# Performance work log

Hardware: AMD Instinct MI355X
Metric: run time of the kernel (lower is better)

The kernel has to match this reference:

```python
import jax, jax.numpy as jnp
import numpy as np

EPS = 1e-7  # tf.keras.backend.epsilon()
DEGREE = 5
SCALE_BASE = 1.0
SCALE_LEGENDRE = 1.0


def legendre_basis(x, degree):
    # min/max normalization over the feature axis -> x_norm in [-1, 1]
    x_min = jnp.min(x, axis=-1, keepdims=True)
    x_max = jnp.max(x, axis=-1, keepdims=True)
    x_norm = 2.0 * (x - x_min) / (x_max - x_min + EPS) - 1.0
    polys = [jnp.ones_like(x_norm), x_norm]
    for n in range(2, degree + 1):
        p_n = ((2 * n - 1) * x_norm * polys[-1] - (n - 1) * polys[-2]) / n
        polys.append(p_n)
    return jnp.stack(polys, axis=-1)  # [b, i, degree+1]


def setup_inputs() -> dict:
    key = jax.random.key(0)
    k1, k2, k3 = jax.random.split(key, 3)
    b, i, o, d = 4096, 1024, 1024, DEGREE + 1
    x = jax.random.normal(k1, (b, i), dtype=jnp.float32)
    # HeUniform: limit = sqrt(6 / fan_in)
    lim_b = np.sqrt(6.0 / i)
    base_weight = jax.random.uniform(k2, (i, o), dtype=jnp.float32, minval=-lim_b, maxval=lim_b)
    legendre_weight = jax.random.uniform(k3, (i, o, d), dtype=jnp.float32, minval=-lim_b, maxval=lim_b)
    return {"x": x, "base_weight": base_weight, "legendre_weight": legendre_weight}


def reference(x, base_weight, legendre_weight):
    base_output = jax.nn.silu(x @ base_weight)  # [b, o]
    basis = legendre_basis(x, DEGREE)  # [b, i, d]
    # 'bi,iod,bid->bo' == fold x into the basis then contract (i, d)
    xb = x[..., None] * basis  # [b, i, d]
    legendre_output = jnp.einsum('bid,iod->bo', xb, legendre_weight)
    return SCALE_BASE * base_output + SCALE_LEGENDRE * legendre_output
```

## Files before the change

### kernel.cpp

```cpp
#include <hip/hip_runtime.h>
#include <stdint.h>

typedef unsigned short u16;
typedef unsigned int   u32;
typedef __attribute__((ext_vector_type(8)))  short bhalf8;
typedef __attribute__((ext_vector_type(16))) float f32x16;

#define B_ROWS 4096
#define I_DIM  1024
#define O_DIM  1024
#define N_D    6
#define K_LEG  (I_DIM * N_D)

#define BM 256
#define BN 256
#define BK 32
#define NU 56
#define SLOT_BYTES 32768
#define LDS_BYTES  131072

__device__ __forceinline__ u16 f2b(float f) {
  u32 u = __float_as_uint(f);
  return (u16)((u + 0x7fffu + ((u >> 16) & 1u)) >> 16);
}

__device__ __forceinline__ void gld_lds16(const void* g, void* l) {
  __builtin_amdgcn_global_load_lds(
      (const __attribute__((address_space(1))) u32*)(uintptr_t)g,
      (__attribute__((address_space(3))) u32*)(u32)(uintptr_t)l, 16, 0, 0);
}

#define RS 201
__global__ void k_prep_w(const float* __restrict__ bw, const float* __restrict__ lw,
                         u16* __restrict__ Bb, u16* __restrict__ Bl) {
  __shared__ float t[32 * RS];
  if (blockIdx.x < 1024) {
    const int bx = blockIdx.x & 31, by = blockIdx.x >> 5;
    const int i0 = by * 32, o0 = bx * 32;
    const int c = threadIdx.x & 31, r0 = threadIdx.x >> 5;
    #pragma unroll
    for (int k = 0; k < 4; ++k) {
      int r = r0 + k * 8;
      t[r * 33 + c] = bw[(size_t)(i0 + r) * O_DIM + o0 + c];
    }
    __syncthreads();
    #pragma unroll
    for (int k = 0; k < 4; ++k) {
      int r = r0 + k * 8;
      Bb[(size_t)(o0 + r) * I_DIM + i0 + c] = f2b(t[c * 33 + r]);
    }
  } else {
    const int blk = blockIdx.x - 1024;
    const int bx = blk & 31, by = blk >> 5;
    const int i0 = by * 32, o0 = bx * 32;
    for (int q = threadIdx.x; q < 32 * 48; q += 256) {
      int ri = q / 48, s4 = q % 48;
      float4 v = *(const float4*)(lw + (size_t)(i0 + ri) * (O_DIM * N_D) + o0 * N_D + s4 * 4);
      float* p = t + ri * RS + s4 * 4;
      p[0] = v.x; p[1] = v.y; p[2] = v.z; p[3] = v.w;
    }
    __syncthreads();
    for (int q = threadIdx.x; q < 32 * 96; q += 256) {
      int ro = q / 96, k = q % 96;
      int e0 = 2 * k, e1 = 2 * k + 1;
      float v0 = t[(e0 / 6) * RS + ro * 6 + (e0 % 6)];
      float v1 = t[(e1 / 6) * RS + ro * 6 + (e1 % 6)];
      u32* dst = (u32*)(Bl + (size_t)(o0 + ro) * K_LEG + i0 * N_D);
      dst[k] = (u32)f2b(v0) | ((u32)f2b(v1) << 16);
    }
  }
}

__global__ void k_prep_basis(const float* __restrict__ x,
                             u16* __restrict__ Ab, u16* __restrict__ Al) {
  int b = blockIdx.x;
  int t = threadIdx.x;
  float4 v = ((const float4*)(x + (size_t)b * I_DIM))[t];
  float mn = fminf(fminf(v.x, v.y), fminf(v.z, v.w));
  float mx = fmaxf(fmaxf(v.x, v.y), fmaxf(v.z, v.w));
  #pragma unroll
  for (int off = 32; off > 0; off >>= 1) {
    mn = fminf(mn, __shfl_xor(mn, off, 64));
    mx = fmaxf(mx, __shfl_xor(mx, off, 64));
  }
  __shared__ float smn[4], smx[4];
  if ((t & 63) == 0) { smn[t >> 6] = mn; smx[t >> 6] = mx; }
  __syncthreads();
  mn = fminf(fminf(smn[0], smn[1]), fminf(smn[2], smn[3]));
  mx = fmaxf(fmaxf(smx[0], smx[1]), fmaxf(smx[2], smx[3]));
  float sc = 2.0f / (mx - mn + 1e-7f);

  float xs[4] = {v.x, v.y, v.z, v.w};
  u32 lb[12];
  #pragma unroll
  for (int e = 0; e < 4; ++e) {
    float xv = xs[e];
    float xn = (xv - mn) * sc - 1.0f;
    float p0 = 1.0f, p1 = xn;
    float p2 = (3.0f * xn * p1 - 1.0f * p0) * (1.0f / 2.0f);
    float p3 = (5.0f * xn * p2 - 2.0f * p1) * (1.0f / 3.0f);
    float p4 = (7.0f * xn * p3 - 3.0f * p2) * (1.0f / 4.0f);
    float p5 = (9.0f * xn * p4 - 4.0f * p3) * (1.0f / 5.0f);
    lb[e * 3 + 0] = (u32)f2b(xv * p0) | ((u32)f2b(xv * p1) << 16);
    lb[e * 3 + 1] = (u32)f2b(xv * p2) | ((u32)f2b(xv * p3) << 16);
    lb[e * 3 + 2] = (u32)f2b(xv * p4) | ((u32)f2b(xv * p5) << 16);
  }
  u32 a0 = (u32)f2b(xs[0]) | ((u32)f2b(xs[1]) << 16);
  u32 a1 = (u32)f2b(xs[2]) | ((u32)f2b(xs[3]) << 16);
  *(uint2*)(Ab + (size_t)b * I_DIM + t * 4) = make_uint2(a0, a1);
  uint4* dl = (uint4*)(Al + (size_t)b * K_LEG + t * 24);
  dl[0] = make_uint4(lb[0], lb[1], lb[2], lb[3]);
  dl[1] = make_uint4(lb[4], lb[5], lb[6], lb[7]);
  dl[2] = make_uint4(lb[8], lb[9], lb[10], lb[11]);
}

__global__ __launch_bounds__(512, 2) void k_gemm(
    const u16* __restrict__ Ab, const u16* __restrict__ Bb,
    const u16* __restrict__ Al, const u16* __restrict__ Bl,
    float* __restrict__ out, float* __restrict__ P) {
  extern __shared__ char lds[];

  const int tid  = threadIdx.x;
  const int wave = tid >> 6;
  const int lane = tid & 63;
  const int wm = wave >> 2;
  const int wn = wave & 3;
  const u32 lr = lane & 31;
  const u32 hi = (u32)lane >> 5;

  const int bid   = blockIdx.x;
  const int bx    = bid >> 4;
  const int by    = (bid >> 2) & 3;
  const int split = bid & 3;
  const size_t brow = (size_t)bx * BM;
  const size_t bcol = (size_t)by * BN;
  const bool s0 = (split == 0);
  const int legbase = s0 ? 0 : (24 + 56 * (split - 1));

  const int r4 = tid >> 2;
  const size_t cs = (size_t)((((tid & 3) ^ ((r4 >> 1) & 3))) * 8);
  char* const l0 = lds + (u32)wave * 1024;

  const u16 *gA0, *gA1, *gB0, *gB1;
  auto set_ptrs = [&](const u16* A, const u16* Bt, size_t ldk, size_t kt) {
    const size_t ko = kt * BK + cs;
    gA0 = A  + (brow + r4) * ldk + ko;
    gA1 = A  + (brow + 128 + r4) * ldk + ko;
    gB0 = Bt + (bcol + r4) * ldk + ko;
    gB1 = Bt + (bcol + 128 + r4) * ldk + ko;
  };
  if (s0) set_ptrs(Ab, Bb, I_DIM, 0);
  else    set_ptrs(Al, Bl, K_LEG, (size_t)legbase);

  const u32 sxor   = (lr >> 1) & 3;
  const u32 chunk0 = ((0 + hi) ^ sxor) * 16;
  const u32 chunk1 = ((2 + hi) ^ sxor) * 16;
  const u32 abase_r = (u32)wm * 8192 + lr * 64;
  const u32 bbase_r = 16384u + ((u32)wn >> 1) * 8192 + ((u32)wn & 1) * 4096 + lr * 64;

  f32x16 acc[4][2] = {};
  bhalf8 af_[4], bf_[2];

  #pragma unroll
  for (int v = 0; v < 3; ++v) {
    char* d = l0 + (size_t)v * SLOT_BYTES;
    gld_lds16(gA0, d);          gld_lds16(gA1, d + 8192);
    gld_lds16(gB0, d + 16384);  gld_lds16(gB1, d + 24576);
    gA0 += BK; gA1 += BK; gB0 += BK; gB1 += BK;
  }
  asm volatile("s_waitcnt vmcnt(8)" ::: "memory");
  __builtin_amdgcn_s_barrier();

#define PH0(u, DO_STAGE) do {                                                 \
    const char* p_ = lds + (size_t)((u) & 3) * SLOT_BYTES;                    \
    _Pragma("unroll")                                                         \
    for (int n = 0; n < 2; ++n) bf_[n] = *(const bhalf8*)(p_ + bbase_r + n * 2048 + chunk0); \
    _Pragma("unroll")                                                         \
    for (int m = 0; m < 4; ++m) af_[m] = *(const bhalf8*)(p_ + abase_r + m * 2048 + chunk0); \
    if (DO_STAGE) {                                                           \
      char* d_ = l0 + (size_t)(((u) + 3) & 3) * SLOT_BYTES;                   \
      gld_lds16(gA0, d_); gld_lds16(gA1, d_ + 8192);                          \
    }                                                                         \
    asm volatile("" ::: "memory");                                            \
    __builtin_amdgcn_s_barrier();                                             \
    asm volatile("s_waitcnt lgkmcnt(0)" ::: "memory");                        \
    __builtin_amdgcn_sched_barrier(0);                                        \
    __builtin_amdgcn_s_setprio(1);                                            \
    _Pragma("unroll")                                                         \
    for (int m = 0; m < 4; ++m)                                               \
      _Pragma("unroll")                                                       \
      for (int n = 0; n < 2; ++n)                                             \
        acc[m][n] = __builtin_amdgcn_mfma_f32_32x32x16_bf16(af_[m], bf_[n], acc[m][n], 0, 0, 0); \
    __builtin_amdgcn_s_setprio(0);                                            \
    __builtin_amdgcn_s_barrier();                                             \
  } while (0)

#define PH1(u, DO_STAGE, VM) do {                                             \
    const char* p_ = lds + (size_t)((u) & 3) * SLOT_BYTES;                    \
    _Pragma("unroll")                                                         \
    for (int n = 0; n < 2; ++n) bf_[n] = *(const bhalf8*)(p_ + bbase_r + n * 2048 + chunk1); \
    _Pragma("unroll")                                                         \
    for (int m = 0; m < 4; ++m) af_[m] = *(const bhalf8*)(p_ + abase_r + m * 2048 + chunk1); \
    if (DO_STAGE) {                                                           \
      char* d_ = l0 + (size_t)(((u) + 3) & 3) * SLOT_BYTES;                   \
      gld_lds16(gB0, d_ + 16384); gld_lds16(gB1, d_ + 24576);                 \
      if (s0 && (u) + 4 == 32) set_ptrs(Al, Bl, K_LEG, 0);                    \
      else { gA0 += BK; gA1 += BK; gB0 += BK; gB1 += BK; }                    \
    }                                                                         \
    asm volatile("s_waitcnt vmcnt(" #VM ")" ::: "memory");                    \
    __builtin_amdgcn_s_barrier();                                             \
    asm volatile("s_waitcnt lgkmcnt(0)" ::: "memory");                        \
    __builtin_amdgcn_sched_barrier(0);                                        \
    __builtin_amdgcn_s_setprio(1);                                            \
    _Pragma("unroll")                                                         \
    for (int m = 0; m < 4; ++m)                                               \
      _Pragma("unroll")                                                       \
      for (int n = 0; n < 2; ++n)                                             \
        acc[m][n] = __builtin_amdgcn_mfma_f32_32x32x16_bf16(af_[m], bf_[n], acc[m][n], 0, 0, 0); \
    __builtin_amdgcn_s_setprio(0);                                            \
    __builtin_amdgcn_s_barrier();                                             \
  } while (0)

  for (int u = 0; u < NU - 3; ++u) {
    if (s0 && u == 32) {
      #pragma unroll
      for (int m = 0; m < 4; ++m)
        #pragma unroll
        for (int n = 0; n < 2; ++n)
          #pragma unroll
          for (int j = 0; j < 16; ++j) {
            float v = acc[m][n][j];
            acc[m][n][j] = v / (1.0f + __expf(-v));
          }
    }
    PH0(u, true);
    PH1(u, true, 8);
  }
  PH0(53, false); PH1(53, false, 4);
  PH0(54, false); PH1(54, false, 0);
  PH0(55, false); PH1(55, false, 0);
#undef PH0
#undef PH1

  float* dst = s0 ? out : (P + (size_t)(split - 1) * ((size_t)B_ROWS * O_DIM));
  #pragma unroll
  for (int m = 0; m < 4; ++m)
    #pragma unroll
    for (int n = 0; n < 2; ++n) {
      const size_t rb = brow + wm * 128 + m * 32 + 4 * hi;
      const size_t c  = bcol + wn * 64 + n * 32 + lr;
      #pragma unroll
      for (int j = 0; j < 16; ++j) {
        const size_t r = rb + (j & 3) + 8 * (j >> 2);
        dst[r * O_DIM + c] = acc[m][n][j];
      }
    }
}

__global__ void k_reduce(float* __restrict__ out, const float* __restrict__ P) {
  const size_t i = (size_t)blockIdx.x * 256 + threadIdx.x;
  const size_t NE = (size_t)B_ROWS * O_DIM / 4;
  float4 a = ((const float4*)out)[i];
  float4 b = ((const float4*)P)[i];
  float4 c = ((const float4*)P)[i + NE];
  float4 d = ((const float4*)P)[i + 2 * NE];
  a.x += b.x + c.x + d.x;  a.y += b.y + c.y + d.y;
  a.z += b.z + c.z + d.z;  a.w += b.w + c.w + d.w;
  ((float4*)out)[i] = a;
}

extern "C" void kernel_launch(void* const* d_in, const int* in_sizes, int n_in,
                              void* d_out, int out_size, void* d_ws, size_t ws_size,
                              hipStream_t stream) {
  const float* x  = (const float*)d_in[0];
  const float* bw = (const float*)d_in[1];
  const float* lw = (const float*)d_in[2];
  float* out = (float*)d_out;

  char* w = (char*)d_ws;
  u16*  Ab = (u16*)(w);
  u16*  Al = (u16*)(w + (size_t)8   * 1024 * 1024);
  u16*  Bb = (u16*)(w + (size_t)56  * 1024 * 1024);
  u16*  Bl = (u16*)(w + (size_t)58  * 1024 * 1024);
  float* P = (float*)(w + (size_t)72 * 1024 * 1024);

  hipFuncSetAttribute((const void*)k_gemm,
                      hipFuncAttributeMaxDynamicSharedMemorySize, LDS_BYTES);

  k_prep_w    <<<dim3(2048), 256, 0, stream>>>(bw, lw, Bb, Bl);
  k_prep_basis<<<dim3(B_ROWS), 256, 0, stream>>>(x, Ab, Al);
  k_gemm      <<<dim3(4 * (B_ROWS / BM) * (O_DIM / BN)), 512, LDS_BYTES, stream>>>(Ab, Bb, Al, Bl, out, P);
  k_reduce    <<<dim3((B_ROWS * O_DIM / 4) / 256), 256, 0, stream>>>(out, P);
}
```

Measured before the change: 118.1 us.

## Software-pipeline LDS fragment loads with MFMA and change LDS swizzle

Restructures the GEMM main loop so the LDS fragment reads for the next half-step overlap the MFMAs of the current half-step, using double-buffered register fragments. It drops from four barriers per K-tile to one, and cuts the global prefetch depth from three stages to two. The LDS XOR swizzle key now also mixes in higher row bits, to reduce bank conflicts on the fragment reads. The shallower prefetch gives global loads less time to hide latency, and the correctness of the single-barrier slot reuse depends on the four-slot ring spacing.

After: 114.9 us. 1.03x faster.

```diff
diff --git a/kernel.cpp b/kernel.cpp
--- a/kernel.cpp
+++ b/kernel.cpp
@@ -138,7 +138,8 @@
   const int legbase = s0 ? 0 : (24 + 56 * (split - 1));
 
   const int r4 = tid >> 2;
-  const size_t cs = (size_t)((((tid & 3) ^ ((r4 >> 1) & 3))) * 8);
+  const u32 skey = (((u32)r4 >> 1) & 3) ^ (((u32)r4 >> 3) & 3);
+  const size_t cs = (size_t)(((u32)(tid & 3) ^ skey) * 8);
   char* const l0 = lds + (u32)wave * 1024;
 
   const u16 *gA0, *gA1, *gB0, *gB1;
@@ -152,76 +153,35 @@
   if (s0) set_ptrs(Ab, Bb, I_DIM, 0);
   else    set_ptrs(Al, Bl, K_LEG, (size_t)legbase);
 
-  const u32 sxor   = (lr >> 1) & 3;
-  const u32 chunk0 = ((0 + hi) ^ sxor) * 16;
-  const u32 chunk1 = ((2 + hi) ^ sxor) * 16;
-  const u32 abase_r = (u32)wm * 8192 + lr * 64;
-  const u32 bbase_r = 16384u + ((u32)wn >> 1) * 8192 + ((u32)wn & 1) * 4096 + lr * 64;
-
-  f32x16 acc[4][2] = {};
-  bhalf8 af_[4], bf_[2];
-
-  #pragma unroll
-  for (int v = 0; v < 3; ++v) {
-    char* d = l0 + (size_t)v * SLOT_BYTES;
+  auto stage = [&](int v) {
+    if (s0 && v == 32) set_ptrs(Al, Bl, K_LEG, 0);
+    char* d = l0 + (size_t)(v & 3) * SLOT_BYTES;
     gld_lds16(gA0, d);          gld_lds16(gA1, d + 8192);
     gld_lds16(gB0, d + 16384);  gld_lds16(gB1, d + 24576);
     gA0 += BK; gA1 += BK; gB0 += BK; gB1 += BK;
-  }
-  asm volatile("s_waitcnt vmcnt(8)" ::: "memory");
+  };
+
+  const u32 key = ((lr >> 1) & 3) ^ ((lr >> 3) & 3);
+  const u32 c00 = ((0 + hi) ^ key) * 16;
+  const u32 c10 = ((2 + hi) ^ key) * 16;
+  const u32 abase_r = (u32)wm * 8192 + lr * 64;
+  const u32 bbase_r = 16384u + ((u32)wn >> 1) * 8192 + ((u32)wn & 1) * 4096 + lr * 64;
+
+  f32x16 acc[4][2] = {};
+  bhalf8 af0[4], bf0[2], af1[4], bf1[2];
+
+  stage(0); stage(1);
+  asm volatile("s_waitcnt vmcnt(4)" ::: "memory");
   __builtin_amdgcn_s_barrier();
-
-#define PH0(u, DO_STAGE) do {                                                 \
-    const char* p_ = lds + (size_t)((u) & 3) * SLOT_BYTES;                    \
-    _Pragma("unroll")                                                         \
-    for (int n = 0; n < 2; ++n) bf_[n] = *(const bhalf8*)(p_ + bbase_r + n * 2048 + chunk0); \
-    _Pragma("unroll")                                                         \
-    for (int m = 0; m < 4; ++m) af_[m] = *(const bhalf8*)(p_ + abase_r + m * 2048 + chunk0); \
-    if (DO_STAGE) {                                                           \
-      char* d_ = l0 + (size_t)(((u) + 3) & 3) * SLOT_BYTES;                   \
-      gld_lds16(gA0, d_); gld_lds16(gA1, d_ + 8192);                          \
-    }                                                                         \
-    asm volatile("" ::: "memory");                                            \
-    __builtin_amdgcn_s_barrier();                                             \
-    asm volatile("s_waitcnt lgkmcnt(0)" ::: "memory");                        \
-    __builtin_amdgcn_sched_barrier(0);                                        \
-    __builtin_amdgcn_s_setprio(1);                                            \
-    _Pragma("unroll")                                                         \
-    for (int m = 0; m < 4; ++m)                                               \
-      _Pragma("unroll")                                                       \
-      for (int n = 0; n < 2; ++n)                                             \
-        acc[m][n] = __builtin_amdgcn_mfma_f32_32x32x16_bf16(af_[m], bf_[n], acc[m][n], 0, 0, 0); \
-    __builtin_amdgcn_s_setprio(0);                                            \
-    __builtin_amdgcn_s_barrier();                                             \
-  } while (0)
-
-#define PH1(u, DO_STAGE, VM) do {                                             \
-    const char* p_ = lds + (size_t)((u) & 3) * SLOT_BYTES;                    \
-    _Pragma("unroll")                                                         \
-    for (int n = 0; n < 2; ++n) bf_[n] = *(const bhalf8*)(p_ + bbase_r + n * 2048 + chunk1); \
-    _Pragma("unroll")                                                         \
-    for (int m = 0; m < 4; ++m) af_[m] = *(const bhalf8*)(p_ + abase_r + m * 2048 + chunk1); \
-    if (DO_STAGE) {                                                           \
-      char* d_ = l0 + (size_t)(((u) + 3) & 3) * SLOT_BYTES;                   \
-      gld_lds16(gB0, d_ + 16384); gld_lds16(gB1, d_ + 24576);                 \
-      if (s0 && (u) + 4 == 32) set_ptrs(Al, Bl, K_LEG, 0);                    \
-      else { gA0 += BK; gA1 += BK; gB0 += BK; gB1 += BK; }                    \
-    }                                                                         \
-    asm volatile("s_waitcnt vmcnt(" #VM ")" ::: "memory");                    \
-    __builtin_amdgcn_s_barrier();                                             \
-    asm volatile("s_waitcnt lgkmcnt(0)" ::: "memory");                        \
-    __builtin_amdgcn_sched_barrier(0);                                        \
-    __builtin_amdgcn_s_setprio(1);                                            \
-    _Pragma("unroll")                                                         \
-    for (int m = 0; m < 4; ++m)                                               \
-      _Pragma("unroll")                                                       \
-      for (int n = 0; n < 2; ++n)                                             \
-        acc[m][n] = __builtin_amdgcn_mfma_f32_32x32x16_bf16(af_[m], bf_[n], acc[m][n], 0, 0, 0); \
-    __builtin_amdgcn_s_setprio(0);                                            \
-    __builtin_amdgcn_s_barrier();                                             \
-  } while (0)
-
-  for (int u = 0; u < NU - 3; ++u) {
+  {
+    const char* p = lds;
+    #pragma unroll
+    for (int n = 0; n < 2; ++n) bf0[n] = *(const bhalf8*)(p + bbase_r + n * 2048 + c00);
+    #pragma unroll
+    for (int m = 0; m < 4; ++m) af0[m] = *(const bhalf8*)(p + abase_r + m * 2048 + c00);
+  }
+
+  for (int u = 0; u < NU; ++u) {
     if (s0 && u == 32) {
       #pragma unroll
       for (int m = 0; m < 4; ++m)
@@ -233,14 +193,50 @@
             acc[m][n][j] = v / (1.0f + __expf(-v));
           }
     }
-    PH0(u, true);
-    PH1(u, true, 8);
-  }
-  PH0(53, false); PH1(53, false, 4);
-  PH0(54, false); PH1(54, false, 0);
-  PH0(55, false); PH1(55, false, 0);
-#undef PH0
-#undef PH1
+    if (u < NU - 2) {
+      stage(u + 2);
+      asm volatile("s_waitcnt vmcnt(4)" ::: "memory");
+    } else {
+      asm volatile("s_waitcnt vmcnt(0)" ::: "memory");
+    }
+    __builtin_amdgcn_s_barrier();
+    asm volatile("s_waitcnt lgkmcnt(0)" ::: "memory");
+    __builtin_amdgcn_sched_barrier(0);
+
+    const char* p = lds + (size_t)(u & 3) * SLOT_BYTES;
+    #pragma unroll
+    for (int n = 0; n < 2; ++n) bf1[n] = *(const bhalf8*)(p + bbase_r + n * 2048 + c10);
+    #pragma unroll
+    for (int m = 0; m < 4; ++m) af1[m] = *(const bhalf8*)(p + abase_r + m * 2048 + c10);
+    __builtin_amdgcn_sched_barrier(0);
+
+    __builtin_amdgcn_s_setprio(1);
+    #pragma unroll
+    for (int m = 0; m < 4; ++m)
+      #pragma unroll
+      for (int n = 0; n < 2; ++n)
+        acc[m][n] = __builtin_amdgcn_mfma_f32_32x32x16_bf16(af0[m], bf0[n], acc[m][n], 0, 0, 0);
+    __builtin_amdgcn_s_setprio(0);
+
+    asm volatile("s_waitcnt lgkmcnt(0)" ::: "memory");
+    __builtin_amdgcn_sched_barrier(0);
+    if (u < NU - 1) {
+      const char* pn = lds + (size_t)((u + 1) & 3) * SLOT_BYTES;
+      #pragma unroll
+      for (int n = 0; n < 2; ++n) bf0[n] = *(const bhalf8*)(pn + bbase_r + n * 2048 + c00);
+      #pragma unroll
+      for (int m = 0; m < 4; ++m) af0[m] = *(const bhalf8*)(pn + abase_r + m * 2048 + c00);
+    }
+    __builtin_amdgcn_sched_barrier(0);
+
+    __builtin_amdgcn_s_setprio(1);
+    #pragma unroll
+    for (int m = 0; m < 4; ++m)
+      #pragma unroll
+      for (int n = 0; n < 2; ++n)
+        acc[m][n] = __builtin_amdgcn_mfma_f32_32x32x16_bf16(af1[m], bf1[n], acc[m][n], 0, 0, 0);
+    __builtin_amdgcn_s_setprio(0);
+  }
 
   float* dst = s0 ? out : (P + (size_t)(split - 1) * ((size_t)B_ROWS * O_DIM));
   #pragma unroll
```
